# Kernel tuning notes

Hardware: AMD Instinct MI355X
Metric: run time of the kernel (lower is better)

## Reference

```python
import jax, jax.numpy as jnp
import numpy as np

NB_HEAD = 16
SIZE_PER_HEAD = 64
D_MODEL = NB_HEAD * SIZE_PER_HEAD  # 1024
B, L = 2, 2048
NEG_BIG = 1e12


def setup_inputs() -> dict:
    key = jax.random.key(0)
    ks = jax.random.split(key, 8)
    return {
        "Q_seq": jax.random.normal(ks[0], (B, L, D_MODEL), dtype=jnp.float32),
        "K_seq": jax.random.normal(ks[1], (B, L, D_MODEL), dtype=jnp.float32),
        "V_seq": jax.random.normal(ks[2], (B, L, D_MODEL), dtype=jnp.float32),
        "q_len": jax.random.randint(ks[3], (B, 1), 1, L, dtype=jnp.int32),
        "v_len": jax.random.randint(ks[4], (B, 1), 1, L, dtype=jnp.int32),
        "WQ": jax.random.normal(ks[5], (D_MODEL, D_MODEL), dtype=jnp.float32) * 0.02,
        "WK": jax.random.normal(ks[6], (D_MODEL, D_MODEL), dtype=jnp.float32) * 0.02,
        "WV": jax.random.normal(ks[7], (D_MODEL, D_MODEL), dtype=jnp.float32) * 0.02,
    }


def _len_mask(lens, length, dtype):
    # Keras code: mask = 1 - cumsum(one_hot(len, L)) -> 1 for pos < len, 0 otherwise
    return (jnp.arange(length)[None, :] < lens).astype(dtype)  # [B, L]


def reference(Q_seq, K_seq, V_seq, q_len, v_len, WQ, WK, WV):
    Bq, Lq, _ = Q_seq.shape
    Lk = K_seq.shape[1]
    # QKV projections, split heads: [B, H, L, D]
    q = (Q_seq @ WQ).reshape(Bq, Lq, NB_HEAD, SIZE_PER_HEAD).transpose(0, 2, 1, 3)
    k = (K_seq @ WK).reshape(Bq, Lk, NB_HEAD, SIZE_PER_HEAD).transpose(0, 2, 1, 3)
    v = (V_seq @ WV).reshape(Bq, Lk, NB_HEAD, SIZE_PER_HEAD).transpose(0, 2, 1, 3)
    # scaled dot-product scores [B, H, Lq, Lk]
    scores = jnp.einsum("bhqd,bhkd->bhqk", q, k) / np.float32(SIZE_PER_HEAD ** 0.5)
    # additive key-length mask (V_len), matching Mask(..., 'add')
    kmask = _len_mask(v_len, Lk, scores.dtype)  # [B, Lk]
    scores = scores - (1.0 - kmask)[:, None, None, :] * np.float32(NEG_BIG)
    A = jax.nn.softmax(scores, axis=-1)
    # attention output, merge heads: [B, Lq, H*D]
    O = jnp.einsum("bhqk,bhkd->bqhd", A, v).reshape(Bq, Lq, D_MODEL)
    # multiplicative query-length mask (Q_len), matching Mask(..., 'mul')
    qmask = _len_mask(q_len, Lq, O.dtype)  # [B, Lq]
    return O * qmask[:, :, None]
```

## Files before the change

kernel.cpp:

```cpp
#include <hip/hip_runtime.h>
#include <cstddef>

#define NB_HEAD 16
#define HEAD_DIM 64
#define D_MODEL 1024
#define BATCH 2
#define SEQ 2048
#define MROWS (BATCH * SEQ)

typedef __bf16 bf16x8 __attribute__((ext_vector_type(8)));
typedef __bf16 bf16x4 __attribute__((ext_vector_type(4)));
typedef float  f32x4  __attribute__((ext_vector_type(4)));

#define XEL ((size_t)MROWS * D_MODEL)
#define WEL ((size_t)D_MODEL * D_MODEL)

static __device__ __forceinline__ size_t xchunk(int row, int k) {
    return ((size_t)(row >> 4) * 32 + (k >> 5)) * 512 + ((k >> 3) & 3) * 128 + (row & 15) * 8 + (k & 7);
}
static __device__ __forceinline__ size_t qkbase(int bh, int row16, int dc) {
    return ((size_t)(bh * 128 + row16) * 2 + dc) * 512;
}
static __device__ __forceinline__ size_t qkelem(int bh, int row, int d) {
    return qkbase(bh, row >> 4, d >> 5) + ((d >> 3) & 3) * 128 + (row & 15) * 8 + (d & 7);
}
static __device__ __forceinline__ size_t vbase(int bh, int d16, int kc) {
    return ((size_t)(bh * 4 + d16) * 64 + kc) * 512;
}
static __device__ __forceinline__ size_t velem(int bh, int d, int key) {
    return vbase(bh, d >> 4, key >> 5) + ((key >> 3) & 3) * 128 + (d & 15) * 8 + (key & 7);
}

static __device__ __forceinline__ void split_bf16(float x, __bf16& h, __bf16& l) {
    h = (__bf16)x;
    l = (__bf16)(x - (float)h);
}

static __device__ __forceinline__ void gload_lds16(const __bf16* g, __bf16* l) {
    __builtin_amdgcn_global_load_lds((const __attribute__((address_space(1))) void*)g,
                                     (__attribute__((address_space(3))) void*)l,
                                     16, 0, 0);
}

__global__ __launch_bounds__(256) void conv_wt_kernel(
    const float* __restrict__ W0, const float* __restrict__ W1,
    const float* __restrict__ W2,
    __bf16* __restrict__ hi, __bf16* __restrict__ lo)
{
    __shared__ float tile[64][65];
    const int t  = threadIdx.x;
    const int k0 = blockIdx.x * 64;
    const int n0 = blockIdx.y * 64;
    const int z  = blockIdx.z;
    const float* W = (z == 0) ? W0 : ((z == 1) ? W1 : W2);
    __bf16* hz = hi + (size_t)z * WEL;
    __bf16* lz = lo + (size_t)z * WEL;

    #pragma unroll
    for (int p = 0; p < 4; ++p) {
        const int e = (p * 256 + t) * 4;
        const int r = e >> 6, c = e & 63;
        const float4 v = *(const float4*)(W + (size_t)(k0 + r) * D_MODEL + n0 + c);
        tile[r][c] = v.x; tile[r][c + 1] = v.y; tile[r][c + 2] = v.z; tile[r][c + 3] = v.w;
    }
    __syncthreads();
    #pragma unroll
    for (int p = 0; p < 4; ++p) {
        const int e = (p * 256 + t) * 4;
        const int n = e >> 6, kc = e & 63;
        __bf16 h[4], l[4];
        #pragma unroll
        for (int u = 0; u < 4; ++u) split_bf16(tile[kc + u][n], h[u], l[u]);
        const size_t a = xchunk(n0 + n, k0 + kc);
        *(bf16x4*)(hz + a) = (bf16x4){h[0], h[1], h[2], h[3]};
        *(bf16x4*)(lz + a) = (bf16x4){l[0], l[1], l[2], l[3]};
    }
}

__global__ __launch_bounds__(256) void conv_x_kernel(
    const float* __restrict__ X0, const float* __restrict__ X1,
    const float* __restrict__ X2,
    const int* __restrict__ q_len, const int* __restrict__ v_len,
    __bf16* __restrict__ xhi, __bf16* __restrict__ xlo)
{
    const int z = blockIdx.y;
    const size_t e = ((size_t)blockIdx.x * 256 + threadIdx.x) * 8;
    const int l = (int)(e >> 10), k = (int)(e & 1023);
    const int bb = l >> 11, lb = l & (SEQ - 1);
    const int len = (z == 0) ? q_len[bb] : v_len[bb];
    if (lb >= ((len + 127) & ~127)) return;

    const float* X = (z == 0) ? X0 : ((z == 1) ? X1 : X2);
    const float4 v0 = *(const float4*)(X + e);
    const float4 v1 = *(const float4*)(X + e + 4);
    const float xs[8] = {v0.x, v0.y, v0.z, v0.w, v1.x, v1.y, v1.z, v1.w};
    bf16x8 h8, l8;
    #pragma unroll
    for (int u = 0; u < 8; ++u) { __bf16 h_, l_; split_bf16(xs[u], h_, l_); h8[u] = h_; l8[u] = l_; }
    const size_t a = z * XEL + xchunk(l, k);
    *(bf16x8*)(xhi + a) = h8;
    *(bf16x8*)(xlo + a) = l8;
}

__global__ __launch_bounds__(256, 2) void proj_mfma_kernel(
    const __bf16* __restrict__ Xhi, const __bf16* __restrict__ Xlo,
    const __bf16* __restrict__ Wchi, const __bf16* __restrict__ Wclo,
    const int* __restrict__ q_len, const int* __restrict__ v_len,
    __bf16* __restrict__ qch, __bf16* __restrict__ qcl,
    __bf16* __restrict__ kch, __bf16* __restrict__ kcl,
    __bf16* __restrict__ vch, __bf16* __restrict__ vcl)
{
    __shared__ __align__(16) __bf16 lds[2][2][2][8][512];

    const int t    = threadIdx.x;
    const int wave = t >> 6, lane = t & 63;
    const int li   = lane & 15, grp = lane >> 4;
    const int wm   = wave >> 1, wn = wave & 1;
    const int m0   = blockIdx.x * 128;
    const int n0   = blockIdx.y * 128;
    const int z    = blockIdx.z;
    const int bb   = m0 >> 11;
    const int l0   = m0 & (SEQ - 1);
    const int need = (z == 0) ? q_len[bb] : v_len[bb];
    if (l0 >= need) return;

    const __bf16* Xh = Xhi + z * XEL;
    const __bf16* Xl = Xlo + z * XEL;
    const __bf16* Wh = Wchi + z * WEL;
    const __bf16* Wl = Wclo + z * WEL;

    const __bf16* gsrc = (wave == 0) ? Xh : (wave == 1) ? Xl : (wave == 2) ? Wh : Wl;
    const size_t  cb16 = (size_t)((wave < 2) ? (m0 >> 4) : (n0 >> 4));

    auto STAGE = [&](int buf, int kc) {
        #pragma unroll
        for (int u = 0; u < 8; ++u) {
            const __bf16* g = gsrc + ((cb16 + (size_t)u) * 32 + (size_t)kc) * 512 + (size_t)lane * 8;
            gload_lds16(g, &lds[buf][wm][wn][u][0]);
        }
    };

    f32x4 acc[4][4] = {};

    STAGE(0, 0);
    __syncthreads();

    #pragma unroll 2
    for (int kc = 0; kc < 32; ++kc) {
        const int cur = kc & 1;
        if (kc < 31) STAGE(cur ^ 1, kc + 1);

        bf16x8 ah[4], al4[4], bh4[4], bl4[4];
        #pragma unroll
        for (int i = 0; i < 4; ++i) {
            ah[i]  = *(const bf16x8*)&lds[cur][0][0][(wm << 2) + i][lane * 8];
            al4[i] = *(const bf16x8*)&lds[cur][0][1][(wm << 2) + i][lane * 8];
            bh4[i] = *(const bf16x8*)&lds[cur][1][0][(wn << 2) + i][lane * 8];
            bl4[i] = *(const bf16x8*)&lds[cur][1][1][(wn << 2) + i][lane * 8];
        }
        #pragma unroll
        for (int j = 0; j < 4; ++j) {
            #pragma unroll
            for (int i = 0; i < 4; ++i) {
                acc[i][j] = __builtin_amdgcn_mfma_f32_16x16x32_bf16(ah[i],  bh4[j], acc[i][j], 0, 0, 0);
                acc[i][j] = __builtin_amdgcn_mfma_f32_16x16x32_bf16(ah[i],  bl4[j], acc[i][j], 0, 0, 0);
                acc[i][j] = __builtin_amdgcn_mfma_f32_16x16x32_bf16(al4[i], bh4[j], acc[i][j], 0, 0, 0);
            }
        }
        __syncthreads();
    }

    #pragma unroll
    for (int j = 0; j < 4; ++j) {
        const int cg = n0 + wn * 64 + j * 16 + li;
        const int hd = cg >> 6, d = cg & 63;
        const int bhI = bb * NB_HEAD + hd;
        #pragma unroll
        for (int i = 0; i < 4; ++i) {
            #pragma unroll
            for (int r = 0; r < 4; ++r) {
                const int rg = m0 + wm * 64 + i * 16 + grp * 4 + r;
                const int lg = rg & (SEQ - 1);
                __bf16 h_, l_;
                split_bf16(acc[i][j][r], h_, l_);
                if (z == 0) {
                    const size_t a = qkelem(bhI, lg, d);
                    qch[a] = h_; qcl[a] = l_;
                } else if (z == 1) {
                    const size_t a = qkelem(bhI, lg, d);
                    kch[a] = h_; kcl[a] = l_;
                } else {
                    const size_t a = velem(bhI, d, lg);
                    vch[a] = h_; vcl[a] = l_;
                }
            }
        }
    }
}

__global__ __launch_bounds__(256, 2) void attn_mfma_kernel(
    const __bf16* __restrict__ qch, const __bf16* __restrict__ qcl,
    const __bf16* __restrict__ kch, const __bf16* __restrict__ kcl,
    const __bf16* __restrict__ vch, const __bf16* __restrict__ vcl,
    const int* __restrict__ q_len, const int* __restrict__ v_len,
    float* __restrict__ out)
{
    __shared__ __align__(16) __bf16 Ps[128][72];

    const int t = threadIdx.x;
    const int wq = t >> 6, lane = t & 63;
    const int grp = lane >> 4, li = lane & 15;
    const int hh = blockIdx.x;
    const int q0 = blockIdx.y * 128;
    const int b  = blockIdx.z;
    const int qlen = q_len[b], vlen = v_len[b];
    const int bh = b * NB_HEAD + hh;
    const int qbase = q0 + wq * 32;

    if (qbase >= qlen) {
        const int row = qbase + (lane >> 1), cs = (lane & 1) * 32;
        float* o = out + ((size_t)b * SEQ + row) * D_MODEL + hh * HEAD_DIM + cs;
        const float4 z4 = make_float4(0.f, 0.f, 0.f, 0.f);
        #pragma unroll
        for (int u = 0; u < 8; ++u) *(float4*)(o + u * 4) = z4;
        return;
    }

    bf16x8 qh[2][2], ql[2][2];
    #pragma unroll
    for (int s = 0; s < 2; ++s)
        #pragma unroll
        for (int ks = 0; ks < 2; ++ks) {
            const size_t a = qkbase(bh, (qbase >> 4) + s, ks) + lane * 8;
            qh[s][ks] = *(const bf16x8*)(qch + a);
            ql[s][ks] = *(const bf16x8*)(qcl + a);
        }

    f32x4 O[2][4] = {};
    float m_s[2][4], l_s[2][4];
    #pragma unroll
    for (int s = 0; s < 2; ++s)
        #pragma unroll
        for (int r = 0; r < 4; ++r) { m_s[s][r] = -1e30f; l_s[s][r] = 0.f; }

    const int nkt = (vlen + 63) >> 6;

    for (int tt = 0; tt < nkt; ++tt) {
        const int k0 = tt * 64;

        f32x4 sacc[2][4] = {};
        #pragma unroll
        for (int ks = 0; ks < 2; ++ks) {
            bf16x8 kh_[4], kl_[4];
            #pragma unroll
            for (int j = 0; j < 4; ++j) {
                const size_t a = qkbase(bh, (k0 >> 4) + j, ks) + lane * 8;
                kh_[j] = *(const bf16x8*)(kch + a);
                kl_[j] = *(const bf16x8*)(kcl + a);
            }
            #pragma unroll
            for (int j = 0; j < 4; ++j)
                #pragma unroll
                for (int s = 0; s < 2; ++s) {
                    sacc[s][j] = __builtin_amdgcn_mfma_f32_16x16x32_bf16(qh[s][ks], kh_[j], sacc[s][j], 0, 0, 0);
                    sacc[s][j] = __builtin_amdgcn_mfma_f32_16x16x32_bf16(qh[s][ks], kl_[j], sacc[s][j], 0, 0, 0);
                    sacc[s][j] = __builtin_amdgcn_mfma_f32_16x16x32_bf16(ql[s][ks], kh_[j], sacc[s][j], 0, 0, 0);
                }
        }

        bf16x8 vh_[2][4], vl_[2][4];
        #pragma unroll
        for (int ks = 0; ks < 2; ++ks)
            #pragma unroll
            for (int j = 0; j < 4; ++j) {
                const size_t a = vbase(bh, j, (k0 >> 5) + ks) + lane * 8;
                vh_[ks][j] = *(const bf16x8*)(vch + a);
                vl_[ks][j] = *(const bf16x8*)(vcl + a);
            }

        #pragma unroll
        for (int s = 0; s < 2; ++s) {
            float mx[4] = {-1e30f, -1e30f, -1e30f, -1e30f};
            #pragma unroll
            for (int j = 0; j < 4; ++j) {
                const int key = k0 + j * 16 + li;
                #pragma unroll
                for (int r = 0; r < 4; ++r) {
                    float v = sacc[s][j][r] * 0.125f;
                    if (key >= vlen) v = -1e30f;
                    sacc[s][j][r] = v;
                    mx[r] = fmaxf(mx[r], v);
                }
            }
            #pragma unroll
            for (int r = 0; r < 4; ++r) {
                mx[r] = fmaxf(mx[r], __shfl_xor(mx[r], 1));
                mx[r] = fmaxf(mx[r], __shfl_xor(mx[r], 2));
                mx[r] = fmaxf(mx[r], __shfl_xor(mx[r], 4));
                mx[r] = fmaxf(mx[r], __shfl_xor(mx[r], 8));
            }
            float al[4], sum[4];
            #pragma unroll
            for (int r = 0; r < 4; ++r) {
                const float mn = fmaxf(m_s[s][r], mx[r]);
                al[r] = __expf(m_s[s][r] - mn);
                m_s[s][r] = mn;
                sum[r] = 0.f;
            }
            #pragma unroll
            for (int j = 0; j < 4; ++j)
                #pragma unroll
                for (int r = 0; r < 4; ++r) {
                    const float p = __expf(sacc[s][j][r] - m_s[s][r]);
                    const __bf16 pb = (__bf16)p;
                    sum[r] += (float)pb;
                    Ps[wq * 32 + s * 16 + grp * 4 + r][j * 16 + li] = pb;
                }
            #pragma unroll
            for (int r = 0; r < 4; ++r) {
                sum[r] += __shfl_xor(sum[r], 1);
                sum[r] += __shfl_xor(sum[r], 2);
                sum[r] += __shfl_xor(sum[r], 4);
                sum[r] += __shfl_xor(sum[r], 8);
                l_s[s][r] = l_s[s][r] * al[r] + sum[r];
            }
            #pragma unroll
            for (int j = 0; j < 4; ++j)
                #pragma unroll
                for (int r = 0; r < 4; ++r) O[s][j][r] *= al[r];
        }
        asm volatile("s_waitcnt lgkmcnt(0)" ::: "memory");

        #pragma unroll
        for (int ks = 0; ks < 2; ++ks) {
            bf16x8 pa[2];
            #pragma unroll
            for (int s = 0; s < 2; ++s)
                pa[s] = *(const bf16x8*)&Ps[wq * 32 + s * 16 + li][ks * 32 + grp * 8];
            #pragma unroll
            for (int j = 0; j < 4; ++j)
                #pragma unroll
                for (int s = 0; s < 2; ++s) {
                    O[s][j] = __builtin_amdgcn_mfma_f32_16x16x32_bf16(pa[s], vh_[ks][j], O[s][j], 0, 0, 0);
                    O[s][j] = __builtin_amdgcn_mfma_f32_16x16x32_bf16(pa[s], vl_[ks][j], O[s][j], 0, 0, 0);
                }
        }
    }

    #pragma unroll
    for (int s = 0; s < 2; ++s)
        #pragma unroll
        for (int r = 0; r < 4; ++r) {
            const int q = qbase + s * 16 + grp * 4 + r;
            const float inv = (q < qlen) ? 1.f / l_s[s][r] : 0.f;
            #pragma unroll
            for (int j = 0; j < 4; ++j)
                out[((size_t)b * SEQ + q) * D_MODEL + hh * HEAD_DIM + j * 16 + li] = O[s][j][r] * inv;
        }
}

extern "C" void kernel_launch(void* const* d_in, const int* in_sizes, int n_in,
                              void* d_out, int out_size, void* d_ws, size_t ws_size,
                              hipStream_t stream)
{
    (void)in_sizes; (void)n_in; (void)out_size; (void)ws_size;
    const float* Q_seq = (const float*)d_in[0];
    const float* K_seq = (const float*)d_in[1];
    const float* V_seq = (const float*)d_in[2];
    const int*   q_len = (const int*)d_in[3];
    const int*   v_len = (const int*)d_in[4];
    const float* WQ    = (const float*)d_in[5];
    const float* WK    = (const float*)d_in[6];
    const float* WV    = (const float*)d_in[7];
    float* out = (float*)d_out;

    __bf16* wchi = (__bf16*)d_ws;
    __bf16* wclo = wchi + 3 * WEL;
    __bf16* xhi_ = wclo + 3 * WEL;
    __bf16* xlo_ = xhi_ + 3 * XEL;
    __bf16* qch_ = xlo_ + 3 * XEL;
    __bf16* qcl_ = qch_ + XEL;
    __bf16* kch_ = qcl_ + XEL;
    __bf16* kcl_ = kch_ + XEL;
    __bf16* vch_ = kcl_ + XEL;
    __bf16* vcl_ = vch_ + XEL;

    dim3 blk(256);

    dim3 cg(D_MODEL / 64, D_MODEL / 64, 3);
    conv_wt_kernel<<<cg, blk, 0, stream>>>(WQ, WK, WV, wchi, wclo);

    dim3 xg((unsigned)(XEL / 2048), 3);
    conv_x_kernel<<<xg, blk, 0, stream>>>(Q_seq, K_seq, V_seq, q_len, v_len, xhi_, xlo_);

    dim3 pg(MROWS / 128, D_MODEL / 128, 3);
    proj_mfma_kernel<<<pg, blk, 0, stream>>>(xhi_, xlo_, wchi, wclo, q_len, v_len,
                                             qch_, qcl_, kch_, kcl_, vch_, vcl_);

    dim3 ag(NB_HEAD, SEQ / 128, BATCH);
    attn_mfma_kernel<<<ag, blk, 0, stream>>>(qch_, qcl_, kch_, kcl_, vch_, vcl_,
                                             q_len, v_len, out);
}
```

Before: 284.4 us.

## Stage K/V tiles in shared memory with double-buffered async loads

After: 331.3 us. 16.5% more time.

```diff
diff --git a/kernel.cpp b/kernel.cpp
--- a/kernel.cpp
+++ b/kernel.cpp
@@ -205,7 +205,8 @@
     const int* __restrict__ q_len, const int* __restrict__ v_len,
     float* __restrict__ out)
 {
-    __shared__ __align__(16) __bf16 Ps[128][72];
+    __shared__ __align__(16) __bf16 KV[2][16][512];
+    __shared__ __align__(16) __bf16 Ps[128][40];
 
     const int t = threadIdx.x;
     const int wq = t >> 6, lane = t & 63;
@@ -217,7 +218,7 @@
     const int bh = b * NB_HEAD + hh;
     const int qbase = q0 + wq * 32;
 
-    if (qbase >= qlen) {
+    if (q0 >= qlen) {
         const int row = qbase + (lane >> 1), cs = (lane & 1) * 32;
         float* o = out + ((size_t)b * SEQ + row) * D_MODEL + hh * HEAD_DIM + cs;
         const float4 z4 = make_float4(0.f, 0.f, 0.f, 0.f);
@@ -225,6 +226,7 @@
         for (int u = 0; u < 8; ++u) *(float4*)(o + u * 4) = z4;
         return;
     }
+    const bool active = (qbase < qlen);
 
     bf16x8 qh[2][2], ql[2][2];
     #pragma unroll
@@ -243,108 +245,121 @@
         #pragma unroll
         for (int r = 0; r < 4; ++r) { m_s[s][r] = -1e30f; l_s[s][r] = 0.f; }
 
-    const int nkt = (vlen + 63) >> 6;
+    const int nkt = (vlen + 31) >> 5;
+
+    auto STAGE = [&](int buf, int tt) {
+        const int k0 = tt * 32;
+        #pragma unroll
+        for (int u = 0; u < 4; ++u) {
+            const int c = wq * 4 + u;
+            const __bf16* g;
+            if (c < 8) {
+                const int ks = c >> 2, j = (c >> 1) & 1;
+                const __bf16* base = (c & 1) ? kcl : kch;
+                g = base + qkbase(bh, (k0 >> 4) + j, ks) + (size_t)lane * 8;
+            } else {
+                const int j = (c >> 1) & 3;
+                const __bf16* base = (c & 1) ? vcl : vch;
+                g = base + vbase(bh, j, k0 >> 5) + (size_t)lane * 8;
+            }
+            gload_lds16(g, &KV[buf][c][0]);
+        }
+    };
+
+    STAGE(0, 0);
+    __syncthreads();
 
     for (int tt = 0; tt < nkt; ++tt) {
-        const int k0 = tt * 64;
-
-        f32x4 sacc[2][4] = {};
-        #pragma unroll
-        for (int ks = 0; ks < 2; ++ks) {
-            bf16x8 kh_[4], kl_[4];
+        const int cur = tt & 1;
+        if (tt + 1 < nkt) STAGE(cur ^ 1, tt + 1);
+
+        if (active) {
+            const int k0 = tt * 32;
+
+            f32x4 sacc[2][2] = {};
+            #pragma unroll
+            for (int ks = 0; ks < 2; ++ks)
+                #pragma unroll
+                for (int j = 0; j < 2; ++j) {
+                    const bf16x8 kh_ = *(const bf16x8*)&KV[cur][ks * 4 + j * 2 + 0][lane * 8];
+                    const bf16x8 kl_ = *(const bf16x8*)&KV[cur][ks * 4 + j * 2 + 1][lane * 8];
+                    #pragma unroll
+                    for (int s = 0; s < 2; ++s) {
+                        sacc[s][j] = __builtin_amdgcn_mfma_f32_16x16x32_bf16(qh[s][ks], kh_, sacc[s][j], 0, 0, 0);
+                        sacc[s][j] = __builtin_amdgcn_mfma_f32_16x16x32_bf16(qh[s][ks], kl_, sacc[s][j], 0, 0, 0);
+                        sacc[s][j] = __builtin_amdgcn_mfma_f32_16x16x32_bf16(ql[s][ks], kh_, sacc[s][j], 0, 0, 0);
+                    }
+                }
+
+            #pragma unroll
+            for (int s = 0; s < 2; ++s) {
+                float mx[4] = {-1e30f, -1e30f, -1e30f, -1e30f};
+                #pragma unroll
+                for (int j = 0; j < 2; ++j) {
+                    const int key = k0 + j * 16 + li;
+                    #pragma unroll
+                    for (int r = 0; r < 4; ++r) {
+                        float v = sacc[s][j][r] * 0.125f;
+                        if (key >= vlen) v = -1e30f;
+                        sacc[s][j][r] = v;
+                        mx[r] = fmaxf(mx[r], v);
+                    }
+                }
+                #pragma unroll
+                for (int r = 0; r < 4; ++r) {
+                    mx[r] = fmaxf(mx[r], __shfl_xor(mx[r], 1));
+                    mx[r] = fmaxf(mx[r], __shfl_xor(mx[r], 2));
+                    mx[r] = fmaxf(mx[r], __shfl_xor(mx[r], 4));
+                    mx[r] = fmaxf(mx[r], __shfl_xor(mx[r], 8));
+                }
+                float al[4], sum[4];
+                #pragma unroll
+                for (int r = 0; r < 4; ++r) {
+                    const float mn = fmaxf(m_s[s][r], mx[r]);
+                    al[r] = __expf(m_s[s][r] - mn);
+                    m_s[s][r] = mn;
+                    sum[r] = 0.f;
+                }
+                #pragma unroll
+                for (int j = 0; j < 2; ++j)
+                    #pragma unroll
+                    for (int r = 0; r < 4; ++r) {
+                        const float p = __expf(sacc[s][j][r] - m_s[s][r]);
+                        const __bf16 pb = (__bf16)p;
+                        sum[r] += (float)pb;
+                        Ps[wq * 32 + s * 16 + grp * 4 + r][j * 16 + li] = pb;
+                    }
+                #pragma unroll
+                for (int r = 0; r < 4; ++r) {
+                    sum[r] += __shfl_xor(sum[r], 1);
+                    sum[r] += __shfl_xor(sum[r], 2);
+                    sum[r] += __shfl_xor(sum[r], 4);
+                    sum[r] += __shfl_xor(sum[r], 8);
+                    l_s[s][r] = l_s[s][r] * al[r] + sum[r];
+                }
+                #pragma unroll
+                for (int j = 0; j < 4; ++j)
+                    #pragma unroll
+                    for (int r = 0; r < 4; ++r) O[s][j][r] *= al[r];
+            }
+            asm volatile("s_waitcnt lgkmcnt(0)" ::: "memory");
+
+            bf16x8 pa[2];
+            #pragma unroll
+            for (int s = 0; s < 2; ++s)
+                pa[s] = *(const bf16x8*)&Ps[wq * 32 + s * 16 + li][grp * 8];
             #pragma unroll
             for (int j = 0; j < 4; ++j) {
-                const size_t a = qkbase(bh, (k0 >> 4) + j, ks) + lane * 8;
-                kh_[j] = *(const bf16x8*)(kch + a);
-                kl_[j] = *(const bf16x8*)(kcl + a);
+                const bf16x8 vh_ = *(const bf16x8*)&KV[cur][8 + j * 2 + 0][lane * 8];
+                const bf16x8 vl_ = *(const bf16x8*)&KV[cur][8 + j * 2 + 1][lane * 8];
+                #pragma unroll
+                for (int s = 0; s < 2; ++s) {
+                    O[s][j] = __builtin_amdgcn_mfma_f32_16x16x32_bf16(pa[s], vh_, O[s][j], 0, 0, 0);
+                    O[s][j] = __builtin_amdgcn_mfma_f32_16x16x32_bf16(pa[s], vl_, O[s][j], 0, 0, 0);
+                }
             }
-            #pragma unroll
-            for (int j = 0; j < 4; ++j)
-                #pragma unroll
-                for (int s = 0; s < 2; ++s) {
-                    sacc[s][j] = __builtin_amdgcn_mfma_f32_16x16x32_bf16(qh[s][ks], kh_[j], sacc[s][j], 0, 0, 0);
-                    sacc[s][j] = __builtin_amdgcn_mfma_f32_16x16x32_bf16(qh[s][ks], kl_[j], sacc[s][j], 0, 0, 0);
-                    sacc[s][j] = __builtin_amdgcn_mfma_f32_16x16x32_bf16(ql[s][ks], kh_[j], sacc[s][j], 0, 0, 0);
-                }
-        }
-
-        bf16x8 vh_[2][4], vl_[2][4];
-        #pragma unroll
-        for (int ks = 0; ks < 2; ++ks)
-            #pragma unroll
-            for (int j = 0; j < 4; ++j) {
-                const size_t a = vbase(bh, j, (k0 >> 5) + ks) + lane * 8;
-                vh_[ks][j] = *(const bf16x8*)(vch + a);
-                vl_[ks][j] = *(const bf16x8*)(vcl + a);
-            }
-
-        #pragma unroll
-        for (int s = 0; s < 2; ++s) {
-            float mx[4] = {-1e30f, -1e30f, -1e30f, -1e30f};
-            #pragma unroll
-            for (int j = 0; j < 4; ++j) {
-                const int key = k0 + j * 16 + li;
-                #pragma unroll
-                for (int r = 0; r < 4; ++r) {
-                    float v = sacc[s][j][r] * 0.125f;
-                    if (key >= vlen) v = -1e30f;
-                    sacc[s][j][r] = v;
-                    mx[r] = fmaxf(mx[r], v);
-                }
-            }
-            #pragma unroll
-            for (int r = 0; r < 4; ++r) {
-                mx[r] = fmaxf(mx[r], __shfl_xor(mx[r], 1));
-                mx[r] = fmaxf(mx[r], __shfl_xor(mx[r], 2));
-                mx[r] = fmaxf(mx[r], __shfl_xor(mx[r], 4));
-                mx[r] = fmaxf(mx[r], __shfl_xor(mx[r], 8));
-            }
-            float al[4], sum[4];
-            #pragma unroll
-            for (int r = 0; r < 4; ++r) {
-                const float mn = fmaxf(m_s[s][r], mx[r]);
-                al[r] = __expf(m_s[s][r] - mn);
-                m_s[s][r] = mn;
-                sum[r] = 0.f;
-            }
-            #pragma unroll
-            for (int j = 0; j < 4; ++j)
-                #pragma unroll
-                for (int r = 0; r < 4; ++r) {
-                    const float p = __expf(sacc[s][j][r] - m_s[s][r]);
-                    const __bf16 pb = (__bf16)p;
-                    sum[r] += (float)pb;
-                    Ps[wq * 32 + s * 16 + grp * 4 + r][j * 16 + li] = pb;
-                }
-            #pragma unroll
-            for (int r = 0; r < 4; ++r) {
-                sum[r] += __shfl_xor(sum[r], 1);
-                sum[r] += __shfl_xor(sum[r], 2);
-                sum[r] += __shfl_xor(sum[r], 4);
-                sum[r] += __shfl_xor(sum[r], 8);
-                l_s[s][r] = l_s[s][r] * al[r] + sum[r];
-            }
-            #pragma unroll
-            for (int j = 0; j < 4; ++j)
-                #pragma unroll
-                for (int r = 0; r < 4; ++r) O[s][j][r] *= al[r];
-        }
-        asm volatile("s_waitcnt lgkmcnt(0)" ::: "memory");
-
-        #pragma unroll
-        for (int ks = 0; ks < 2; ++ks) {
-            bf16x8 pa[2];
-            #pragma unroll
-            for (int s = 0; s < 2; ++s)
-                pa[s] = *(const bf16x8*)&Ps[wq * 32 + s * 16 + li][ks * 32 + grp * 8];
-            #pragma unroll
-            for (int j = 0; j < 4; ++j)
-                #pragma unroll
-                for (int s = 0; s < 2; ++s) {
-                    O[s][j] = __builtin_amdgcn_mfma_f32_16x16x32_bf16(pa[s], vh_[ks][j], O[s][j], 0, 0, 0);
-                    O[s][j] = __builtin_amdgcn_mfma_f32_16x16x32_bf16(pa[s], vl_[ks][j], O[s][j], 0, 0, 0);
-                }
-        }
+        }
+        __syncthreads();
     }
 
     #pragma unroll
```

## Split attention over key range with a merge pass; narrow projection tiles

Applied to the files above, without the earlier changes.

After: 275.2 us. 3.3% less time.

```diff
diff --git a/kernel.cpp b/kernel.cpp
--- a/kernel.cpp
+++ b/kernel.cpp
@@ -7,6 +7,7 @@
 #define BATCH 2
 #define SEQ 2048
 #define MROWS (BATCH * SEQ)
+#define NSPLIT 2
 
 typedef __bf16 bf16x8 __attribute__((ext_vector_type(8)));
 typedef __bf16 bf16x4 __attribute__((ext_vector_type(4)));
@@ -102,7 +103,7 @@
     *(bf16x8*)(xlo + a) = l8;
 }
 
-__global__ __launch_bounds__(256, 2) void proj_mfma_kernel(
+__global__ __launch_bounds__(256, 3) void proj_mfma_kernel(
     const __bf16* __restrict__ Xhi, const __bf16* __restrict__ Xlo,
     const __bf16* __restrict__ Wchi, const __bf16* __restrict__ Wclo,
     const int* __restrict__ q_len, const int* __restrict__ v_len,
@@ -110,14 +111,14 @@
     __bf16* __restrict__ kch, __bf16* __restrict__ kcl,
     __bf16* __restrict__ vch, __bf16* __restrict__ vcl)
 {
-    __shared__ __align__(16) __bf16 lds[2][2][2][8][512];
+    __shared__ __align__(16) __bf16 lds[2][24][512];
 
     const int t    = threadIdx.x;
     const int wave = t >> 6, lane = t & 63;
     const int li   = lane & 15, grp = lane >> 4;
     const int wm   = wave >> 1, wn = wave & 1;
     const int m0   = blockIdx.x * 128;
-    const int n0   = blockIdx.y * 128;
+    const int n0   = blockIdx.y * 64;
     const int z    = blockIdx.z;
     const int bb   = m0 >> 11;
     const int l0   = m0 & (SEQ - 1);
@@ -129,18 +130,26 @@
     const __bf16* Wh = Wchi + z * WEL;
     const __bf16* Wl = Wclo + z * WEL;
 
-    const __bf16* gsrc = (wave == 0) ? Xh : (wave == 1) ? Xl : (wave == 2) ? Wh : Wl;
-    const size_t  cb16 = (size_t)((wave < 2) ? (m0 >> 4) : (n0 >> 4));
+    const __bf16* gs[6];
+    #pragma unroll
+    for (int u = 0; u < 6; ++u) {
+        const int c = u * 4 + wave;
+        const __bf16* src;
+        int idx;
+        if (c < 8)       { src = Xh; idx = (m0 >> 4) + c; }
+        else if (c < 16) { src = Xl; idx = (m0 >> 4) + (c - 8); }
+        else if (c < 20) { src = Wh; idx = (n0 >> 4) + (c - 16); }
+        else             { src = Wl; idx = (n0 >> 4) + (c - 20); }
+        gs[u] = src + (size_t)idx * 32 * 512 + (size_t)lane * 8;
+    }
 
     auto STAGE = [&](int buf, int kc) {
         #pragma unroll
-        for (int u = 0; u < 8; ++u) {
-            const __bf16* g = gsrc + ((cb16 + (size_t)u) * 32 + (size_t)kc) * 512 + (size_t)lane * 8;
-            gload_lds16(g, &lds[buf][wm][wn][u][0]);
-        }
+        for (int u = 0; u < 6; ++u)
+            gload_lds16(gs[u] + (size_t)kc * 512, &lds[buf][u * 4 + wave][0]);
     };
 
-    f32x4 acc[4][4] = {};
+    f32x4 acc[4][2] = {};
 
     STAGE(0, 0);
     __syncthreads();
@@ -150,29 +159,32 @@
         const int cur = kc & 1;
         if (kc < 31) STAGE(cur ^ 1, kc + 1);
 
-        bf16x8 ah[4], al4[4], bh4[4], bl4[4];
+        bf16x8 ah[4], al4[4], bh2[2], bl2[2];
         #pragma unroll
         for (int i = 0; i < 4; ++i) {
-            ah[i]  = *(const bf16x8*)&lds[cur][0][0][(wm << 2) + i][lane * 8];
-            al4[i] = *(const bf16x8*)&lds[cur][0][1][(wm << 2) + i][lane * 8];
-            bh4[i] = *(const bf16x8*)&lds[cur][1][0][(wn << 2) + i][lane * 8];
-            bl4[i] = *(const bf16x8*)&lds[cur][1][1][(wn << 2) + i][lane * 8];
-        }
-        #pragma unroll
-        for (int j = 0; j < 4; ++j) {
+            ah[i]  = *(const bf16x8*)&lds[cur][(wm << 2) + i][lane * 8];
+            al4[i] = *(const bf16x8*)&lds[cur][8 + (wm << 2) + i][lane * 8];
+        }
+        #pragma unroll
+        for (int j = 0; j < 2; ++j) {
+            bh2[j] = *(const bf16x8*)&lds[cur][16 + (wn << 1) + j][lane * 8];
+            bl2[j] = *(const bf16x8*)&lds[cur][20 + (wn << 1) + j][lane * 8];
+        }
+        #pragma unroll
+        for (int j = 0; j < 2; ++j) {
             #pragma unroll
             for (int i = 0; i < 4; ++i) {
-                acc[i][j] = __builtin_amdgcn_mfma_f32_16x16x32_bf16(ah[i],  bh4[j], acc[i][j], 0, 0, 0);
-                acc[i][j] = __builtin_amdgcn_mfma_f32_16x16x32_bf16(ah[i],  bl4[j], acc[i][j], 0, 0, 0);
-                acc[i][j] = __builtin_amdgcn_mfma_f32_16x16x32_bf16(al4[i], bh4[j], acc[i][j], 0, 0, 0);
+                acc[i][j] = __builtin_amdgcn_mfma_f32_16x16x32_bf16(ah[i],  bh2[j], acc[i][j], 0, 0, 0);
+                acc[i][j] = __builtin_amdgcn_mfma_f32_16x16x32_bf16(ah[i],  bl2[j], acc[i][j], 0, 0, 0);
+                acc[i][j] = __builtin_amdgcn_mfma_f32_16x16x32_bf16(al4[i], bh2[j], acc[i][j], 0, 0, 0);
             }
         }
         __syncthreads();
     }
 
     #pragma unroll
-    for (int j = 0; j < 4; ++j) {
-        const int cg = n0 + wn * 64 + j * 16 + li;
+    for (int j = 0; j < 2; ++j) {
+        const int cg = n0 + wn * 32 + j * 16 + li;
         const int hd = cg >> 6, d = cg & 63;
         const int bhI = bb * NB_HEAD + hd;
         #pragma unroll
@@ -203,7 +215,7 @@
     const __bf16* __restrict__ kch, const __bf16* __restrict__ kcl,
     const __bf16* __restrict__ vch, const __bf16* __restrict__ vcl,
     const int* __restrict__ q_len, const int* __restrict__ v_len,
-    float* __restrict__ out)
+    float* __restrict__ Opart, float* __restrict__ Mbuf, float* __restrict__ Lbuf)
 {
     __shared__ __align__(16) __bf16 Ps[128][72];
 
@@ -211,20 +223,14 @@
     const int wq = t >> 6, lane = t & 63;
     const int grp = lane >> 4, li = lane & 15;
     const int hh = blockIdx.x;
-    const int q0 = blockIdx.y * 128;
+    const int split = blockIdx.y & (NSPLIT - 1);
+    const int q0 = (blockIdx.y >> 1) * 128;
     const int b  = blockIdx.z;
     const int qlen = q_len[b], vlen = v_len[b];
     const int bh = b * NB_HEAD + hh;
     const int qbase = q0 + wq * 32;
 
-    if (qbase >= qlen) {
-        const int row = qbase + (lane >> 1), cs = (lane & 1) * 32;
-        float* o = out + ((size_t)b * SEQ + row) * D_MODEL + hh * HEAD_DIM + cs;
-        const float4 z4 = make_float4(0.f, 0.f, 0.f, 0.f);
-        #pragma unroll
-        for (int u = 0; u < 8; ++u) *(float4*)(o + u * 4) = z4;
-        return;
-    }
+    if (qbase >= qlen) return;
 
     bf16x8 qh[2][2], ql[2][2];
     #pragma unroll
@@ -243,9 +249,12 @@
         #pragma unroll
         for (int r = 0; r < 4; ++r) { m_s[s][r] = -1e30f; l_s[s][r] = 0.f; }
 
-    const int nkt = (vlen + 63) >> 6;
-
-    for (int tt = 0; tt < nkt; ++tt) {
+    const int nktT = (vlen + 63) >> 6;
+    const int half = (nktT + NSPLIT - 1) / NSPLIT;
+    const int tBeg = split * half;
+    const int tEnd = (nktT < tBeg + half) ? nktT : (tBeg + half);
+
+    for (int tt = tBeg; tt < tEnd; ++tt) {
         const int k0 = tt * 64;
 
         f32x4 sacc[2][4] = {};
@@ -347,16 +356,53 @@
         }
     }
 
+    const size_t osplit = (size_t)split * MROWS * D_MODEL;
     #pragma unroll
     for (int s = 0; s < 2; ++s)
         #pragma unroll
         for (int r = 0; r < 4; ++r) {
             const int q = qbase + s * 16 + grp * 4 + r;
-            const float inv = (q < qlen) ? 1.f / l_s[s][r] : 0.f;
-            #pragma unroll
-            for (int j = 0; j < 4; ++j)
-                out[((size_t)b * SEQ + q) * D_MODEL + hh * HEAD_DIM + j * 16 + li] = O[s][j][r] * inv;
-        }
+            if (q < qlen) {
+                #pragma unroll
+                for (int j = 0; j < 4; ++j)
+                    Opart[osplit + ((size_t)b * SEQ + q) * D_MODEL + hh * HEAD_DIM + j * 16 + li] = O[s][j][r];
+                if (li == 0) {
+                    const size_t mi = (((size_t)split * BATCH + b) * NB_HEAD + hh) * SEQ + q;
+                    Mbuf[mi] = m_s[s][r];
+                    Lbuf[mi] = l_s[s][r];
+                }
+            }
+        }
+}
+
+__global__ __launch_bounds__(256) void attn_merge_kernel(
+    const float* __restrict__ Opart, const float* __restrict__ Mbuf,
+    const float* __restrict__ Lbuf, const int* __restrict__ q_len,
+    float* __restrict__ out)
+{
+    const int row = blockIdx.x;
+    const int b = row >> 11, q = row & (SEQ - 1);
+    const int col = threadIdx.x * 4;
+    const int hh = col >> 6;
+    const size_t oidx = (size_t)row * D_MODEL + col;
+
+    float4 o = make_float4(0.f, 0.f, 0.f, 0.f);
+    if (q < q_len[b]) {
+        const size_t mlsz = (size_t)BATCH * NB_HEAD * SEQ;
+        const size_t mi = ((size_t)b * NB_HEAD + hh) * SEQ + q;
+        const float m0 = Mbuf[mi], m1 = Mbuf[mlsz + mi];
+        const float l0 = Lbuf[mi], l1 = Lbuf[mlsz + mi];
+        const float M  = fmaxf(m0, m1);
+        const float w0 = __expf(m0 - M), w1 = __expf(m1 - M);
+        const float inv = 1.f / (l0 * w0 + l1 * w1);
+        const float4 a = *(const float4*)(Opart + oidx);
+        const float4 c = *(const float4*)(Opart + (size_t)MROWS * D_MODEL + oidx);
+        o.x = (a.x * w0 + c.x * w1) * inv;
+        o.y = (a.y * w0 + c.y * w1) * inv;
+        o.z = (a.z * w0 + c.z * w1) * inv;
+        o.w = (a.w * w0 + c.w * w1) * inv;
+    }
+    *(float4*)(out + oidx) = o;
 }
 
 extern "C" void kernel_launch(void* const* d_in, const int* in_sizes, int n_in,
@@ -385,6 +431,10 @@
     __bf16* vch_ = kcl_ + XEL;
     __bf16* vcl_ = vch_ + XEL;
 
+    float* Opart = (float*)xhi_;
+    float* Mbuf  = (float*)wchi;
+    float* Lbuf  = Mbuf + (size_t)NSPLIT * BATCH * NB_HEAD * SEQ;
+
     dim3 blk(256);
 
     dim3 cg(D_MODEL / 64, D_MODEL / 64, 3);
@@ -393,11 +443,13 @@
     dim3 xg((unsigned)(XEL / 2048), 3);
     conv_x_kernel<<<xg, blk, 0, stream>>>(Q_seq, K_seq, V_seq, q_len, v_len, xhi_, xlo_);
 
-    dim3 pg(MROWS / 128, D_MODEL / 128, 3);
+    dim3 pg(MROWS / 128, D_MODEL / 64, 3);
     proj_mfma_kernel<<<pg, blk, 0, stream>>>(xhi_, xlo_, wchi, wclo, q_len, v_len,
                                              qch_, qcl_, kch_, kcl_, vch_, vcl_);
 
-    dim3 ag(NB_HEAD, SEQ / 128, BATCH);
+    dim3 ag(NB_HEAD, (SEQ / 128) * NSPLIT, BATCH);
     attn_mfma_kernel<<<ag, blk, 0, stream>>>(qch_, qcl_, kch_, kcl_, vch_, vcl_,
-                                             q_len, v_len, out);
-}
+                                             q_len, v_len, Opart, Mbuf, Lbuf);
+
+    attn_merge_kernel<<<dim3(MROWS), blk, 0, stream>>>(Opart, Mbuf, Lbuf, q_len, out);
+}
```
